# Optimization experiments

Hardware: AMD Instinct MI355X
Metric: run time of the kernel (lower is better)

Reference implementation:

```python
import jax, jax.numpy as jnp
import numpy as np

VOCAB, EMBED, HIDDEN, NUM_CLASSES, PAD_IDX = 50257, 128, 128, 4, 0
B, T = 256, 512


def setup_inputs() -> dict:
    key = jax.random.key(0)
    ks = jax.random.split(key, 10)
    x = jax.random.randint(ks[0], (B, T), 0, VOCAB)
    h0 = jnp.zeros((B, HIDDEN), dtype=jnp.float32)
    # embedding: uniform(-0.1, 0.1), pad row zeroed (matches init_weights)
    emb = jax.random.uniform(ks[1], (VOCAB, EMBED), jnp.float32, -0.1, 0.1)
    emb = emb.at[PAD_IDX].set(0.0)
    def xavier(k, shape):
        fan_out, fan_in = shape
        bound = float(np.sqrt(6.0 / (fan_in + fan_out)))
        return jax.random.uniform(k, shape, jnp.float32, -bound, bound)
    W_ih = xavier(ks[2], (HIDDEN, EMBED))      # rnn.weight_ih_l0
    W_hh = xavier(ks[3], (HIDDEN, HIDDEN))     # rnn.weight_hh_l0
    b_ih = jnp.zeros((HIDDEN,), jnp.float32)
    b_hh = jnp.zeros((HIDDEN,), jnp.float32)
    W1 = xavier(ks[4], (2 * HIDDEN, HIDDEN))   # output_layer1
    b1 = jnp.zeros((2 * HIDDEN,), jnp.float32)
    W2 = xavier(ks[5], (NUM_CLASSES, 2 * HIDDEN))  # output_layer2
    b2 = jnp.zeros((NUM_CLASSES,), jnp.float32)
    return {"x": x, "h0": h0, "emb": emb, "W_ih": W_ih, "W_hh": W_hh,
            "b_ih": b_ih, "b_hh": b_hh, "W1": W1, "b1": b1, "W2": W2, "b2": b2}


def reference(x, h0, emb, W_ih, W_hh, b_ih, b_hh, W1, b1, W2, b2):
    # Embedding lookup (dropout layers are identity in eval mode)
    embedded = emb[x]                                    # [B, T, E]
    # Precompute input projection for every step, then scan the recurrence.
    x_proj = jnp.einsum('bte,he->bth', embedded, W_ih) + b_ih + b_hh  # [B, T, H]
    x_proj_t = jnp.swapaxes(x_proj, 0, 1)                # [T, B, H]

    def step(h, xp):
        h_new = jnp.tanh(xp + h @ W_hh.T)                # [B, H]
        return h_new, None

    last_hidden, _ = jax.lax.scan(step, h0, x_proj_t)    # [B, H]
    # MLP head: Linear -> ReLU -> Linear
    hidden_mlp = jax.nn.relu(last_hidden @ W1.T + b1)    # [B, 2H]
    logits = hidden_mlp @ W2.T + b2                      # [B, C]
    return (logits, last_hidden)
```

## Files before the change

### kernel.cpp

```cpp
#include <hip/hip_runtime.h>
#include <hip/hip_bf16.h>
#include <math.h>

#define BB 256
#define TT 512
#define EE 128
#define HH 128
#define NC 4
#define MM (BB * TT)

typedef __bf16 bf16x8 __attribute__((ext_vector_type(8)));
typedef __bf16 bf16x4 __attribute__((ext_vector_type(4)));
typedef float  f32x4  __attribute__((ext_vector_type(4)));

__device__ __forceinline__ float fast_tanh(float x) {
    float t = __builtin_amdgcn_exp2f(x * 2.885390081777927f);
    return 1.f - 2.f * __builtin_amdgcn_rcpf(1.f + t);
}

__device__ __forceinline__ void bar_lds() {
    asm volatile("s_waitcnt lgkmcnt(0)\n\ts_barrier" ::: "memory");
}

template <typename XPT>
__global__ __launch_bounds__(256, 3) void embed_gemm(
    const int* __restrict__ x, const float* __restrict__ emb,
    const float* __restrict__ Wih, const float* __restrict__ bih,
    const float* __restrict__ bhh, XPT* __restrict__ xpout)
{
    const int tid = threadIdx.x;
    const int m0  = blockIdx.x * 64;

    const int LDW = 72;
    const int LDE = 132;
    __shared__ __align__(16) char smem[36864 + 512];
    __bf16* Wh     = (__bf16*)smem;
    __bf16* Wl     = (__bf16*)(smem + 18432);
    float*  epi    = (float*)smem;
    float*  bias_s = (float*)(smem + 36864);

    if (tid < 128) bias_s[tid] = bih[tid] + bhh[tid];

    const int lane = tid & 63, wid = tid >> 6;
    const int col  = lane & 15, quad = lane >> 4;

    const int gi = x[m0 + wid * 16 + col];
    const float* arow = emb + (size_t)gi * 128;

    f32x4 acc[8];
#pragma unroll
    for (int nt = 0; nt < 8; ++nt) acc[nt] = f32x4{0.f, 0.f, 0.f, 0.f};

#pragma unroll
    for (int half = 0; half < 2; ++half) {
#pragma unroll
        for (int it = 0; it < 8; ++it) {
            int c   = it * 256 + tid;
            int row = c >> 4;
            int seg = c & 15;
            float4 wv = ((const float4*)Wih)[row * 32 + half * 16 + seg];
            bf16x4 wh, wl;
            wh[0] = (__bf16)wv.x; wl[0] = (__bf16)(wv.x - (float)wh[0]);
            wh[1] = (__bf16)wv.y; wl[1] = (__bf16)(wv.y - (float)wh[1]);
            wh[2] = (__bf16)wv.z; wl[2] = (__bf16)(wv.z - (float)wh[2]);
            wh[3] = (__bf16)wv.w; wl[3] = (__bf16)(wv.w - (float)wh[3]);
            *(bf16x4*)&Wh[row * LDW + seg * 4] = wh;
            *(bf16x4*)&Wl[row * LDW + seg * 4] = wl;
        }
        __syncthreads();

#pragma unroll
        for (int kk = 0; kk < 2; ++kk) {
            const float* ap = arow + half * 64 + kk * 32 + quad * 8;
            f32x4 a0 = *(const f32x4*)ap;
            f32x4 a1 = *(const f32x4*)(ap + 4);
            bf16x8 afh, afl;
#pragma unroll
            for (int u = 0; u < 4; ++u) {
                afh[u]     = (__bf16)a0[u]; afl[u]     = (__bf16)(a0[u] - (float)afh[u]);
                afh[u + 4] = (__bf16)a1[u]; afl[u + 4] = (__bf16)(a1[u] - (float)afh[u + 4]);
            }
#pragma unroll
            for (int nt = 0; nt < 8; ++nt) {
                int ro = (nt * 16 + col) * LDW + kk * 32 + quad * 8;
                bf16x8 wfh = *(const bf16x8*)&Wh[ro];
                bf16x8 wfl = *(const bf16x8*)&Wl[ro];
                acc[nt] = __builtin_amdgcn_mfma_f32_16x16x32_bf16(afh, wfh, acc[nt], 0, 0, 0);
                acc[nt] = __builtin_amdgcn_mfma_f32_16x16x32_bf16(afl, wfh, acc[nt], 0, 0, 0);
                acc[nt] = __builtin_amdgcn_mfma_f32_16x16x32_bf16(afh, wfl, acc[nt], 0, 0, 0);
            }
        }
        __syncthreads();
    }

#pragma unroll
    for (int nt = 0; nt < 8; ++nt) {
        int n = nt * 16 + col;
        float bs = bias_s[n];
#pragma unroll
        for (int r = 0; r < 4; ++r)
            epi[(wid * 16 + quad * 4 + r) * LDE + n] = acc[nt][r] + bs;
    }
    __syncthreads();

#pragma unroll
    for (int it = 0; it < 8; ++it) {
        int c   = it * 256 + tid;
        int row = c >> 5;
        int cf  = c & 31;
        f32x4 v = *(const f32x4*)&epi[row * LDE + cf * 4];
        if (sizeof(XPT) == 4) {
            *(f32x4*)&((float*)xpout)[(size_t)(m0 + row) * 128 + cf * 4] = v;
        } else {
            bf16x4 bv;
            bv[0] = (__bf16)v[0]; bv[1] = (__bf16)v[1];
            bv[2] = (__bf16)v[2]; bv[3] = (__bf16)v[3];
            *(bf16x4*)&((__bf16*)xpout)[(size_t)(m0 + row) * 128 + cf * 4] = bv;
        }
    }
}

template <typename XPT>
__global__ __launch_bounds__(256, 1) void rnn_scan_mlp(
    const XPT* __restrict__ xp, const float* __restrict__ Whh,
    const float* __restrict__ h0, const float* __restrict__ W1,
    const float* __restrict__ b1, const float* __restrict__ W2,
    const float* __restrict__ b2, float* __restrict__ out)
{
    const int b    = blockIdx.x;
    const int tid  = threadIdx.x;
    const int q    = tid >> 6;
    const int lane = tid & 63;
    const int l32  = lane & 31;
    const bool owner = (lane < 32);
    const int o = q * 32 + l32;

    __shared__ float h_priv[4][32];
    __shared__ float part[2][4][128];
    __shared__ float h_full[128];
    __shared__ float hid[256];

    f32x4 wA[8], wB[8];
    {
        const float* r0 = Whh + (size_t)lane * 128 + q * 32;
        const float* r1 = Whh + (size_t)(lane + 64) * 128 + q * 32;
#pragma unroll
        for (int c = 0; c < 8; ++c) {
            wA[c] = *(const f32x4*)(r0 + c * 4);
            wB[c] = *(const f32x4*)(r1 + c * 4);
        }
    }
#pragma unroll
    for (int c = 0; c < 8; ++c)
        asm volatile("" : "+v"(wA[c]), "+v"(wB[c]));

    if (owner) h_priv[q][l32] = h0[b * 128 + o];

    const XPT* xpb = xp + (size_t)b * (TT * 128);
    float xv[8];
#pragma unroll
    for (int s = 0; s < 8; ++s)
        xv[s] = owner ? (float)xpb[s * 128 + o] : 0.f;

    bar_lds();

    for (int tw = 0; tw < TT; tw += 8) {
#pragma unroll
        for (int ts = 0; ts < 8; ++ts) {
            const int p = ts & 1;
            const float* hq = &h_priv[q][0];
            f32x4 h4[8];
#pragma unroll
            for (int u = 0; u < 8; ++u) h4[u] = *(const f32x4*)&hq[u * 4];

            f32x4 aA = f32x4{0.f, 0.f, 0.f, 0.f};
            f32x4 aB = f32x4{0.f, 0.f, 0.f, 0.f};
#pragma unroll
            for (int u = 0; u < 8; ++u) {
                aA += wA[u] * h4[u];
                aB += wB[u] * h4[u];
            }
            part[p][q][lane]      = (aA[0] + aA[1]) + (aA[2] + aA[3]);
            part[p][q][64 + lane] = (aB[0] + aB[1]) + (aB[2] + aB[3]);

            bar_lds();

            if (owner) {
                float s = (part[p][0][o] + part[p][1][o])
                        + (part[p][2][o] + part[p][3][o]);
                float hv = fast_tanh(s + xv[ts]);
                h_priv[q][l32] = hv;
                if (tw + 8 < TT)
                    xv[ts] = (float)xpb[(size_t)(tw + 8 + ts) * 128 + o];
            }
        }
    }

    if (owner) h_full[o] = h_priv[q][l32];
    bar_lds();

    if (tid < 128) out[1024 + b * 128 + tid] = h_full[tid];

    {
        float acc = b1[tid];
        const float4* wrow = (const float4*)(W1 + (size_t)tid * 128);
#pragma unroll
        for (int k4 = 0; k4 < 32; ++k4) {
            float4 wv = wrow[k4];
            acc += wv.x * h_full[k4 * 4 + 0] + wv.y * h_full[k4 * 4 + 1]
                 + wv.z * h_full[k4 * 4 + 2] + wv.w * h_full[k4 * 4 + 3];
        }
        hid[tid] = fmaxf(acc, 0.f);
    }
    __syncthreads();

    float s = 0.f;
#pragma unroll
    for (int qq = 0; qq < 4; ++qq)
        s += hid[qq * 64 + lane] * W2[q * 256 + qq * 64 + lane];
#pragma unroll
    for (int off = 32; off > 0; off >>= 1) s += __shfl_down(s, off);
    if (lane == 0) out[b * 4 + q] = s + b2[q];
}

extern "C" void kernel_launch(void* const* d_in, const int* in_sizes, int n_in,
                              void* d_out, int out_size, void* d_ws, size_t ws_size,
                              hipStream_t stream)
{
    const int*   x   = (const int*)d_in[0];
    const float* h0  = (const float*)d_in[1];
    const float* emb = (const float*)d_in[2];
    const float* Wih = (const float*)d_in[3];
    const float* Whh = (const float*)d_in[4];
    const float* bih = (const float*)d_in[5];
    const float* bhh = (const float*)d_in[6];
    const float* W1  = (const float*)d_in[7];
    const float* b1  = (const float*)d_in[8];
    const float* W2  = (const float*)d_in[9];
    const float* b2  = (const float*)d_in[10];
    float* out = (float*)d_out;

    const size_t xp_f32_bytes = (size_t)MM * 128 * sizeof(float);

    if (ws_size >= xp_f32_bytes) {
        float* xpw = (float*)d_ws;
        embed_gemm<float><<<MM / 64, 256, 0, stream>>>(x, emb, Wih, bih, bhh, xpw);
        rnn_scan_mlp<float><<<BB, 256, 0, stream>>>(xpw, Whh, h0, W1, b1, W2, b2, out);
    } else {
        __bf16* xpw = (__bf16*)d_ws;
        embed_gemm<__bf16><<<MM / 64, 256, 0, stream>>>(x, emb, Wih, bih, bhh, xpw);
        rnn_scan_mlp<__bf16><<<BB, 256, 0, stream>>>(xpw, Whh, h0, W1, b1, W2, b2, out);
    }
}
```

Measured before the change: 285.0 us.

## Fuse embedding input projection into recurrent scan kernel, dropping precomputed xproj buffer

```diff
diff --git a/kernel.cpp b/kernel.cpp
--- a/kernel.cpp
+++ b/kernel.cpp
@@ -7,11 +7,8 @@
 #define EE 128
 #define HH 128
 #define NC 4
-#define MM (BB * TT)
 
-typedef __bf16 bf16x8 __attribute__((ext_vector_type(8)));
-typedef __bf16 bf16x4 __attribute__((ext_vector_type(4)));
-typedef float  f32x4  __attribute__((ext_vector_type(4)));
+typedef float f32x4 __attribute__((ext_vector_type(4)));
 
 __device__ __forceinline__ float fast_tanh(float x) {
     float t = __builtin_amdgcn_exp2f(x * 2.885390081777927f);
@@ -22,107 +19,10 @@
     asm volatile("s_waitcnt lgkmcnt(0)\n\ts_barrier" ::: "memory");
 }
 
-template <typename XPT>
-__global__ __launch_bounds__(256, 3) void embed_gemm(
+__global__ __launch_bounds__(256, 1) void rnn_fused(
     const int* __restrict__ x, const float* __restrict__ emb,
-    const float* __restrict__ Wih, const float* __restrict__ bih,
-    const float* __restrict__ bhh, XPT* __restrict__ xpout)
-{
-    const int tid = threadIdx.x;
-    const int m0  = blockIdx.x * 64;
-
-    const int LDW = 72;
-    const int LDE = 132;
-    __shared__ __align__(16) char smem[36864 + 512];
-    __bf16* Wh     = (__bf16*)smem;
-    __bf16* Wl     = (__bf16*)(smem + 18432);
-    float*  epi    = (float*)smem;
-    float*  bias_s = (float*)(smem + 36864);
-
-    if (tid < 128) bias_s[tid] = bih[tid] + bhh[tid];
-
-    const int lane = tid & 63, wid = tid >> 6;
-    const int col  = lane & 15, quad = lane >> 4;
-
-    const int gi = x[m0 + wid * 16 + col];
-    const float* arow = emb + (size_t)gi * 128;
-
-    f32x4 acc[8];
-#pragma unroll
-    for (int nt = 0; nt < 8; ++nt) acc[nt] = f32x4{0.f, 0.f, 0.f, 0.f};
-
-#pragma unroll
-    for (int half = 0; half < 2; ++half) {
-#pragma unroll
-        for (int it = 0; it < 8; ++it) {
-            int c   = it * 256 + tid;
-            int row = c >> 4;
-            int seg = c & 15;
-            float4 wv = ((const float4*)Wih)[row * 32 + half * 16 + seg];
-            bf16x4 wh, wl;
-            wh[0] = (__bf16)wv.x; wl[0] = (__bf16)(wv.x - (float)wh[0]);
-            wh[1] = (__bf16)wv.y; wl[1] = (__bf16)(wv.y - (float)wh[1]);
-            wh[2] = (__bf16)wv.z; wl[2] = (__bf16)(wv.z - (float)wh[2]);
-            wh[3] = (__bf16)wv.w; wl[3] = (__bf16)(wv.w - (float)wh[3]);
-            *(bf16x4*)&Wh[row * LDW + seg * 4] = wh;
-            *(bf16x4*)&Wl[row * LDW + seg * 4] = wl;
-        }
-        __syncthreads();
-
-#pragma unroll
-        for (int kk = 0; kk < 2; ++kk) {
-            const float* ap = arow + half * 64 + kk * 32 + quad * 8;
-            f32x4 a0 = *(const f32x4*)ap;
-            f32x4 a1 = *(const f32x4*)(ap + 4);
-            bf16x8 afh, afl;
-#pragma unroll
-            for (int u = 0; u < 4; ++u) {
-                afh[u]     = (__bf16)a0[u]; afl[u]     = (__bf16)(a0[u] - (float)afh[u]);
-                afh[u + 4] = (__bf16)a1[u]; afl[u + 4] = (__bf16)(a1[u] - (float)afh[u + 4]);
-            }
-#pragma unroll
-            for (int nt = 0; nt < 8; ++nt) {
-                int ro = (nt * 16 + col) * LDW + kk * 32 + quad * 8;
-                bf16x8 wfh = *(const bf16x8*)&Wh[ro];
-                bf16x8 wfl = *(const bf16x8*)&Wl[ro];
-                acc[nt] = __builtin_amdgcn_mfma_f32_16x16x32_bf16(afh, wfh, acc[nt], 0, 0, 0);
-                acc[nt] = __builtin_amdgcn_mfma_f32_16x16x32_bf16(afl, wfh, acc[nt], 0, 0, 0);
-                acc[nt] = __builtin_amdgcn_mfma_f32_16x16x32_bf16(afh, wfl, acc[nt], 0, 0, 0);
-            }
-        }
-        __syncthreads();
-    }
-
-#pragma unroll
-    for (int nt = 0; nt < 8; ++nt) {
-        int n = nt * 16 + col;
-        float bs = bias_s[n];
-#pragma unroll
-        for (int r = 0; r < 4; ++r)
-            epi[(wid * 16 + quad * 4 + r) * LDE + n] = acc[nt][r] + bs;
-    }
-    __syncthreads();
-
-#pragma unroll
-    for (int it = 0; it < 8; ++it) {
-        int c   = it * 256 + tid;
-        int row = c >> 5;
-        int cf  = c & 31;
-        f32x4 v = *(const f32x4*)&epi[row * LDE + cf * 4];
-        if (sizeof(XPT) == 4) {
-            *(f32x4*)&((float*)xpout)[(size_t)(m0 + row) * 128 + cf * 4] = v;
-        } else {
-            bf16x4 bv;
-            bv[0] = (__bf16)v[0]; bv[1] = (__bf16)v[1];
-            bv[2] = (__bf16)v[2]; bv[3] = (__bf16)v[3];
-            *(bf16x4*)&((__bf16*)xpout)[(size_t)(m0 + row) * 128 + cf * 4] = bv;
-        }
-    }
-}
-
-template <typename XPT>
-__global__ __launch_bounds__(256, 1) void rnn_scan_mlp(
-    const XPT* __restrict__ xp, const float* __restrict__ Whh,
+    const float* __restrict__ Wih, const float* __restrict__ Whh,
+    const float* __restrict__ bih, const float* __restrict__ bhh,
     const float* __restrict__ h0, const float* __restrict__ W1,
     const float* __restrict__ b1, const float* __restrict__ W2,
     const float* __restrict__ b2, float* __restrict__ out)
@@ -137,61 +37,96 @@
 
     __shared__ float h_priv[4][32];
     __shared__ float part[2][4][128];
+    __shared__ float ebuf[2][8][128];
+    __shared__ int   sx[TT];
     __shared__ float h_full[128];
     __shared__ float hid[256];
 
-    f32x4 wA[8], wB[8];
     {
-        const float* r0 = Whh + (size_t)lane * 128 + q * 32;
-        const float* r1 = Whh + (size_t)(lane + 64) * 128 + q * 32;
+        int2 v = ((const int2*)(x + (size_t)b * TT))[tid];
+        *(int2*)&sx[tid * 2] = v;
+    }
+
+    f32x4 wA[8], wB[8], iA[8], iB[8];
+    {
+        const float* hr0 = Whh + (size_t)lane * 128 + q * 32;
+        const float* hr1 = Whh + (size_t)(lane + 64) * 128 + q * 32;
+        const float* ir0 = Wih + (size_t)lane * 128 + q * 32;
+        const float* ir1 = Wih + (size_t)(lane + 64) * 128 + q * 32;
 #pragma unroll
         for (int c = 0; c < 8; ++c) {
-            wA[c] = *(const f32x4*)(r0 + c * 4);
-            wB[c] = *(const f32x4*)(r1 + c * 4);
+            wA[c] = *(const f32x4*)(hr0 + c * 4);
+            wB[c] = *(const f32x4*)(hr1 + c * 4);
+            iA[c] = *(const f32x4*)(ir0 + c * 4);
+            iB[c] = *(const f32x4*)(ir1 + c * 4);
         }
     }
 #pragma unroll
     for (int c = 0; c < 8; ++c)
         asm volatile("" : "+v"(wA[c]), "+v"(wB[c]));
+#pragma unroll
+    for (int c = 0; c < 8; ++c)
+        asm volatile("" : "+v"(iA[c]), "+v"(iB[c]));
 
-    if (owner) h_priv[q][l32] = h0[b * 128 + o];
+    float bs_o = 0.f;
+    if (owner) {
+        bs_o = bih[o] + bhh[o];
+        h_priv[q][l32] = h0[b * 128 + o];
+    }
+    __syncthreads();
 
-    const XPT* xpb = xp + (size_t)b * (TT * 128);
-    float xv[8];
-#pragma unroll
-    for (int s = 0; s < 8; ++s)
-        xv[s] = owner ? (float)xpb[s * 128 + o] : 0.f;
-
+    f32x4 eh0 = f32x4{0.f, 0.f, 0.f, 0.f}, eh1 = eh0;
+    if (owner) {
+        f32x4 e0a = *(const f32x4*)(emb + (size_t)sx[q]      * 128 + l32 * 4);
+        f32x4 e0b = *(const f32x4*)(emb + (size_t)sx[q + 4]  * 128 + l32 * 4);
+        eh0       = *(const f32x4*)(emb + (size_t)sx[q + 8]  * 128 + l32 * 4);
+        eh1       = *(const f32x4*)(emb + (size_t)sx[q + 12] * 128 + l32 * 4);
+        *(f32x4*)&ebuf[0][q][l32 * 4]     = e0a;
+        *(f32x4*)&ebuf[0][q + 4][l32 * 4] = e0b;
+    }
     bar_lds();
 
     for (int tw = 0; tw < TT; tw += 8) {
+        const int wb = (tw >> 3) & 1;
 #pragma unroll
         for (int ts = 0; ts < 8; ++ts) {
             const int p = ts & 1;
             const float* hq = &h_priv[q][0];
-            f32x4 h4[8];
-#pragma unroll
-            for (int u = 0; u < 8; ++u) h4[u] = *(const f32x4*)&hq[u * 4];
-
-            f32x4 aA = f32x4{0.f, 0.f, 0.f, 0.f};
-            f32x4 aB = f32x4{0.f, 0.f, 0.f, 0.f};
+            const float* eq = &ebuf[wb][ts][q * 32];
+            f32x4 aW = f32x4{0.f, 0.f, 0.f, 0.f};
+            f32x4 bW = f32x4{0.f, 0.f, 0.f, 0.f};
+            f32x4 aE = f32x4{0.f, 0.f, 0.f, 0.f};
+            f32x4 bE = f32x4{0.f, 0.f, 0.f, 0.f};
 #pragma unroll
             for (int u = 0; u < 8; ++u) {
-                aA += wA[u] * h4[u];
-                aB += wB[u] * h4[u];
+                f32x4 h4 = *(const f32x4*)&hq[u * 4];
+                f32x4 e4 = *(const f32x4*)&eq[u * 4];
+                aW += wA[u] * h4;
+                bW += wB[u] * h4;
+                aE += iA[u] * e4;
+                bE += iB[u] * e4;
             }
-            part[p][q][lane]      = (aA[0] + aA[1]) + (aA[2] + aA[3]);
-            part[p][q][64 + lane] = (aB[0] + aB[1]) + (aB[2] + aB[3]);
+            f32x4 sA = aW + aE, sB = bW + bE;
+            part[p][q][lane]      = (sA[0] + sA[1]) + (sA[2] + sA[3]);
+            part[p][q][64 + lane] = (sB[0] + sB[1]) + (sB[2] + sB[3]);
+
+            if (ts == 7) {
+                if (tw + 8 < TT && owner) {
+                    *(f32x4*)&ebuf[wb ^ 1][q][l32 * 4]     = eh0;
+                    *(f32x4*)&ebuf[wb ^ 1][q + 4][l32 * 4] = eh1;
+                }
+                if (tw + 16 < TT && owner) {
+                    eh0 = *(const f32x4*)(emb + (size_t)sx[tw + 16 + q]     * 128 + l32 * 4);
+                    eh1 = *(const f32x4*)(emb + (size_t)sx[tw + 16 + 4 + q] * 128 + l32 * 4);
+                }
+            }
 
             bar_lds();
 
             if (owner) {
                 float s = (part[p][0][o] + part[p][1][o])
                         + (part[p][2][o] + part[p][3][o]);
-                float hv = fast_tanh(s + xv[ts]);
-                h_priv[q][l32] = hv;
-                if (tw + 8 < TT)
-                    xv[ts] = (float)xpb[(size_t)(tw + 8 + ts) * 128 + o];
+                h_priv[q][l32] = fast_tanh(s + bs_o);
             }
         }
     }
@@ -240,15 +175,6 @@
     const float* b2  = (const float*)d_in[10];
     float* out = (float*)d_out;
 
-    const size_t xp_f32_bytes = (size_t)MM * 128 * sizeof(float);
-
-    if (ws_size >= xp_f32_bytes) {
-        float* xpw = (float*)d_ws;
-        embed_gemm<float><<<MM / 64, 256, 0, stream>>>(x, emb, Wih, bih, bhh, xpw);
-        rnn_scan_mlp<float><<<BB, 256, 0, stream>>>(xpw, Whh, h0, W1, b1, W2, b2, out);
-    } else {
-        __bf16* xpw = (__bf16*)d_ws;
-        embed_gemm<__bf16><<<MM / 64, 256, 0, stream>>>(x, emb, Wih, bih, bhh, xpw);
-        rnn_scan_mlp<__bf16><<<BB, 256, 0, stream>>>(xpw, Whh, h0, W1, b1, W2, b2, out);
-    }
+    rnn_fused<<<BB, 256, 0, stream>>>(x, emb, Wih, Whh, bih, bhh, h0,
+                                      W1, b1, W2, b2, out);
 }
```

Measured after the change: 317.5 us. 11.4% more time.
